# Optimization experiments

Measured on AMD Instinct MI355X. Metric: run time of the kernel, lower is better.

## Reference

```python
import jax, jax.numpy as jnp
import numpy as np

N, E, DIM, H, EDIM = 50000, 800000, 128, 4, 16
C = DIM // H  # per-head channels = 32

def _ln(x, g, b, eps=1e-5):
    mu = jnp.mean(x, -1, keepdims=True)
    var = jnp.mean((x - mu) ** 2, -1, keepdims=True)
    return (x - mu) * jax.lax.rsqrt(var + eps) * g + b

def setup_inputs() -> dict:
    key = jax.random.key(0)
    ks = jax.random.split(key, 16)
    s = lambda d: 1.0 / np.sqrt(d)
    inp = {
        'x': jax.random.normal(ks[0], (N, DIM), jnp.float32),
        'edge_index_s': jax.random.randint(ks[1], (2, E), 0, N, jnp.int64),
        'edge_attr_s': jax.random.normal(ks[2], (E, EDIM), jnp.float32),
        'Wq': jax.random.normal(ks[3], (DIM, DIM), jnp.float32) * s(DIM),
        'bq': jnp.zeros((DIM,), jnp.float32),
        'Wk': jax.random.normal(ks[4], (DIM, DIM), jnp.float32) * s(DIM),
        'bk': jnp.zeros((DIM,), jnp.float32),
        'Wv': jax.random.normal(ks[5], (DIM, DIM), jnp.float32) * s(DIM),
        'bv': jnp.zeros((DIM,), jnp.float32),
        'We': jax.random.normal(ks[6], (EDIM, DIM), jnp.float32) * s(EDIM),
        'be': jnp.zeros((DIM,), jnp.float32),
        'Ws': jax.random.normal(ks[7], (DIM, DIM), jnp.float32) * s(DIM),
        'bs': jnp.zeros((DIM,), jnp.float32),
        'Wbeta': jax.random.normal(ks[8], (3 * DIM, 1), jnp.float32) * s(3 * DIM),
        'g1': jnp.ones((DIM,), jnp.float32),
        'b1': jnp.zeros((DIM,), jnp.float32),
        'Wf1': jax.random.normal(ks[9], (DIM, 4 * DIM), jnp.float32) * s(DIM),
        'bf1': jnp.zeros((4 * DIM,), jnp.float32),
        'Wf2': jax.random.normal(ks[10], (4 * DIM, DIM), jnp.float32) * s(4 * DIM),
        'bf2': jnp.zeros((DIM,), jnp.float32),
        'g2': jnp.ones((DIM,), jnp.float32),
        'b2': jnp.zeros((DIM,), jnp.float32),
    }
    return inp

def reference(x, edge_index_s, edge_attr_s, Wq, bq, Wk, bk, Wv, bv, We, be,
              Ws, bs, Wbeta, g1, b1, Wf1, bf1, Wf2, bf2, g2, b2):
    src, dst = edge_index_s[0], edge_index_s[1]
    # project + reshape to [N, H, C]
    q = (x @ Wq + bq).reshape(N, H, C)
    k = (x @ Wk + bk).reshape(N, H, C)
    v = (x @ Wv + bv).reshape(N, H, C)
    e = (edge_attr_s @ We + be).reshape(E, H, C)
    # gather along edges (irregular access)
    kj = k[src] + e  # [E, H, C]
    vj = v[src] + e
    alpha = jnp.einsum('ehc,ehc->eh', q[dst], kj) / jnp.sqrt(jnp.float32(C))
    # segment softmax over incoming edges of each dst node
    m = jax.ops.segment_max(alpha, dst, num_segments=N)  # [N, H]
    a = jnp.exp(alpha - m[dst])
    denom = jax.ops.segment_sum(a, dst, num_segments=N)
    a = a / (denom[dst] + 1e-16)
    out = jax.ops.segment_sum(a[:, :, None] * vj, dst, num_segments=N)  # [N, H, C]
    out = out.reshape(N, DIM)
    # beta-gated skip (TransformerConv beta=True)
    xr = x @ Ws + bs
    beta = jax.nn.sigmoid(jnp.concatenate([out, xr, out - xr], -1) @ Wbeta)  # [N, 1]
    xs = beta * xr + (1.0 - beta) * out
    # residual + LN + FFN + LN
    h = _ln(x + xs, g1, b1)
    ff = jax.nn.relu(h @ Wf1 + bf1) @ Wf2 + bf2
    return _ln(h + ff, g2, b2)
```

## Files before the change

### kernel.cpp

```cpp
#include <hip/hip_runtime.h>
#include <hip/hip_bf16.h>

#define NN 50000
#define EE 800000
#define DIMM 128

typedef __attribute__((ext_vector_type(8))) short bf16x8;
typedef __attribute__((ext_vector_type(8))) unsigned short us8;
typedef __attribute__((ext_vector_type(4))) float f32x4;

static __device__ __forceinline__ unsigned short f2bf(float f) {
    unsigned int u = __float_as_uint(f);
    unsigned int r = (u + 0x7fffu + ((u >> 16) & 1u)) >> 16;
    return (unsigned short)r;
}
static __device__ __forceinline__ float bf2f(unsigned short s) {
    return __uint_as_float(((unsigned int)s) << 16);
}

__global__ __launch_bounds__(256) void pack_w(
    const float* __restrict__ Wq, const float* __restrict__ Wk,
    const float* __restrict__ Wv, const float* __restrict__ Ws,
    const float* __restrict__ bq, const float* __restrict__ bk,
    const float* __restrict__ bv, const float* __restrict__ bs,
    const float* __restrict__ Wf1, const float* __restrict__ Wf2,
    unsigned short* __restrict__ wqkvsT, unsigned short* __restrict__ wf1T,
    unsigned short* __restrict__ wf2T, float* __restrict__ biasq)
{
    int i = blockIdx.x * 256 + threadIdx.x;
    if (i < 65536) {
        int n = i >> 7, k = i & 127;
        int sel = n >> 7, col = n & 127;
        const float* W = sel == 0 ? Wq : sel == 1 ? Wk : sel == 2 ? Wv : Ws;
        wqkvsT[i] = f2bf(W[k * 128 + col]);
    } else if (i < 131072) {
        int j = i - 65536; int n = j >> 7, k = j & 127;
        wf1T[j] = f2bf(Wf1[k * 512 + n]);
    } else if (i < 196608) {
        int j = i - 131072; int n = j >> 9, k = j & 511;
        wf2T[j] = f2bf(Wf2[k * 128 + n]);
    } else if (i < 196608 + 512) {
        int j = i - 196608; int sel = j >> 7;
        const float* bp = sel == 0 ? bq : sel == 1 ? bk : sel == 2 ? bv : bs;
        biasq[j] = bp[j & 127];
    }
}

template<bool A_BF16, int EPI>
__global__ __launch_bounds__(256) void gemm_k(
    const void* __restrict__ Ap, const unsigned short* __restrict__ Bt,
    const float* __restrict__ bias, void* __restrict__ Cp,
    float* __restrict__ qb, unsigned short* __restrict__ kvb, float* __restrict__ xrb,
    int M, int Nn, int K)
{
    __shared__ unsigned short As[128][72];
    __shared__ unsigned short Bs[64][72];
    int tid = threadIdx.x;
    int nb = Nn >> 6;
    int bm = blockIdx.x / nb, bn = blockIdx.x % nb;
    int w = tid >> 6, lane = tid & 63;
    int wm = w >> 1, wn = w & 1;
    int lr = lane & 15, quad = lane >> 4;

    f32x4 acc[4][2];
    #pragma unroll
    for (int i = 0; i < 4; i++)
        #pragma unroll
        for (int j = 0; j < 2; j++) { f32x4 z = {0.f, 0.f, 0.f, 0.f}; acc[i][j] = z; }

    for (int kc = 0; kc < K; kc += 64) {
        #pragma unroll
        for (int it = 0; it < 4; ++it) {
            int row = it * 32 + (tid >> 3);
            int k8 = (tid & 7) * 8;
            int rg = bm * 128 + row;
            us8 st = {0, 0, 0, 0, 0, 0, 0, 0};
            if (rg < M) {
                if constexpr (A_BF16) {
                    st = *(const us8*)((const unsigned short*)Ap + (size_t)rg * K + kc + k8);
                } else {
                    const float* src = (const float*)Ap + (size_t)rg * K + kc + k8;
                    float4 f0 = *(const float4*)src;
                    float4 f1 = *(const float4*)(src + 4);
                    st[0] = f2bf(f0.x); st[1] = f2bf(f0.y); st[2] = f2bf(f0.z); st[3] = f2bf(f0.w);
                    st[4] = f2bf(f1.x); st[5] = f2bf(f1.y); st[6] = f2bf(f1.z); st[7] = f2bf(f1.w);
                }
            }
            *(us8*)&As[row][k8] = st;
        }
        {
            int nrow = tid >> 2;
            int k16 = (tid & 3) * 16;
            const unsigned short* src = Bt + (size_t)(bn * 64 + nrow) * K + kc + k16;
            *(us8*)&Bs[nrow][k16]     = *(const us8*)src;
            *(us8*)&Bs[nrow][k16 + 8] = *(const us8*)(src + 8);
        }
        __syncthreads();
        #pragma unroll
        for (int kk = 0; kk < 2; ++kk) {
            bf16x8 af[4], bfr[2];
            #pragma unroll
            for (int mi = 0; mi < 4; mi++)
                af[mi] = *(const bf16x8*)&As[wm * 64 + mi * 16 + lr][kk * 32 + quad * 8];
            #pragma unroll
            for (int ni = 0; ni < 2; ni++)
                bfr[ni] = *(const bf16x8*)&Bs[wn * 32 + ni * 16 + lr][kk * 32 + quad * 8];
            #pragma unroll
            for (int mi = 0; mi < 4; mi++)
                #pragma unroll
                for (int ni = 0; ni < 2; ni++)
                    acc[mi][ni] = __builtin_amdgcn_mfma_f32_16x16x32_bf16(af[mi], bfr[ni], acc[mi][ni], 0, 0, 0);
        }
        __syncthreads();
    }
    #pragma unroll
    for (int mi = 0; mi < 4; mi++) {
        #pragma unroll
        for (int ni = 0; ni < 2; ni++) {
            int cg = bn * 64 + wn * 32 + ni * 16 + lr;
            float bv = bias[cg];
            #pragma unroll
            for (int r = 0; r < 4; r++) {
                int rg = bm * 128 + wm * 64 + mi * 16 + quad * 4 + r;
                if (rg < M) {
                    float val = acc[mi][ni][r] + bv;
                    if constexpr (EPI == 0) {
                        ((float*)Cp)[(size_t)rg * Nn + cg] = val;
                    } else if constexpr (EPI == 1) {
                        val = fmaxf(val, 0.f);
                        ((unsigned short*)Cp)[(size_t)rg * Nn + cg] = f2bf(val);
                    } else {
                        int sel = cg >> 7, c = cg & 127;
                        if (sel == 0)      qb[(size_t)rg * 128 + c] = val;
                        else if (sel == 1) kvb[(size_t)rg * 256 + 2 * c] = f2bf(val);
                        else if (sel == 2) kvb[(size_t)rg * 256 + 2 * c + 1] = f2bf(val);
                        else               xrb[(size_t)rg * 128 + c] = val;
                    }
                }
            }
        }
    }
}

__global__ __launch_bounds__(256) void hist_k(const int* __restrict__ dst, int* __restrict__ deg) {
    int e = blockIdx.x * 256 + threadIdx.x;
    if (e < EE) atomicAdd(&deg[dst[e]], 1);
}

__global__ __launch_bounds__(256) void scan_phaseA(const int* __restrict__ deg, int* __restrict__ rs,
                                                   int* __restrict__ bsum) {
    __shared__ int sm[256];
    int tid = threadIdx.x;
    int i = blockIdx.x * 256 + tid;
    int v = (i < NN) ? deg[i] : 0;
    sm[tid] = v;
    __syncthreads();
    #pragma unroll
    for (int off = 1; off < 256; off <<= 1) {
        int t = 0;
        if (tid >= off) t = sm[tid - off];
        __syncthreads();
        if (tid >= off) sm[tid] += t;
        __syncthreads();
    }
    if (i < NN) rs[i] = sm[tid] - v;
    if (tid == 255) bsum[blockIdx.x] = sm[255];
}

__global__ __launch_bounds__(256) void scan_phaseB(int* __restrict__ bsum, int nb) {
    __shared__ int sm[256];
    int tid = threadIdx.x;
    int v = (tid < nb) ? bsum[tid] : 0;
    sm[tid] = v;
    __syncthreads();
    #pragma unroll
    for (int off = 1; off < 256; off <<= 1) {
        int t = 0;
        if (tid >= off) t = sm[tid - off];
        __syncthreads();
        if (tid >= off) sm[tid] += t;
        __syncthreads();
    }
    if (tid < nb) bsum[tid] = sm[tid] - v;
}

__global__ __launch_bounds__(256) void scan_phaseC(int* __restrict__ rs, const int* __restrict__ bsum) {
    int i = blockIdx.x * 256 + threadIdx.x;
    if (i < NN) rs[i] += bsum[blockIdx.x];
    if (i == 0) rs[NN] = EE;
}

__global__ __launch_bounds__(256) void scatter_k(
    const int* __restrict__ src, const int* __restrict__ dst,
    const float* __restrict__ eattr, const int* __restrict__ rs,
    int* __restrict__ cur, int* __restrict__ srcs_sorted,
    unsigned short* __restrict__ eas)
{
    int e = blockIdx.x * 256 + threadIdx.x;
    if (e < EE) {
        int d = dst[e];
        int p = atomicAdd(&cur[d], 1);
        int pos = rs[d] + p;
        srcs_sorted[pos] = src[e];
        const float* ap = eattr + (size_t)e * 16;
        float4 a0 = *(const float4*)ap;
        float4 a1 = *(const float4*)(ap + 4);
        float4 a2 = *(const float4*)(ap + 8);
        float4 a3 = *(const float4*)(ap + 12);
        us8 lo, hi;
        lo[0] = f2bf(a0.x); lo[1] = f2bf(a0.y); lo[2] = f2bf(a0.z); lo[3] = f2bf(a0.w);
        lo[4] = f2bf(a1.x); lo[5] = f2bf(a1.y); lo[6] = f2bf(a1.z); lo[7] = f2bf(a1.w);
        hi[0] = f2bf(a2.x); hi[1] = f2bf(a2.y); hi[2] = f2bf(a2.z); hi[3] = f2bf(a2.w);
        hi[4] = f2bf(a3.x); hi[5] = f2bf(a3.y); hi[6] = f2bf(a3.z); hi[7] = f2bf(a3.w);
        *(us8*)(eas + (size_t)pos * 16)     = lo;
        *(us8*)(eas + (size_t)pos * 16 + 8) = hi;
    }
}

__global__ __launch_bounds__(256, 3) void attn_kernel(
    const float* __restrict__ q, const unsigned int* __restrict__ kvb,
    const float* __restrict__ xr, const float* __restrict__ x,
    const unsigned short* __restrict__ eas, const int* __restrict__ srcs,
    const int* __restrict__ rs,
    const float* __restrict__ We, const float* __restrict__ be,
    const float* __restrict__ Wbeta, const float* __restrict__ gamma1,
    const float* __restrict__ beta1, float* __restrict__ hout)
{
    int wave = threadIdx.x >> 6;
    int lane = threadIdx.x & 63;
    int n = blockIdx.x * 4 + wave;
    if (n >= NN) return;
    int c0 = lane * 2, c1 = c0 + 1;

    float we0[16], we1[16];
    #pragma unroll
    for (int j = 0; j < 16; j++) { we0[j] = We[j * 128 + c0]; we1[j] = We[j * 128 + c1]; }
    float be0 = be[c0], be1 = be[c1];

    float2 q2 = *(const float2*)(q + (size_t)n * 128 + c0);
    q2.x *= 0.17677669529663687f;
    q2.y *= 0.17677669529663687f;

    float l = 0.f, a0 = 0.f, a1 = 0.f;
    int beg = rs[n], end = rs[n + 1];

    const size_t EAS_MAX = (size_t)EE * 16 - 1;
    float ea_c = bf2f(eas[min((size_t)beg * 16 + lane, EAS_MAX)]);
    int sr_c[4];
    #pragma unroll
    for (int j = 0; j < 4; j++) sr_c[j] = srcs[min(beg + j, EE - 1)];

    for (int g = beg; g < end; g += 4) {
        int cnt = end - g;
        uint2 kvp[4];
        #pragma unroll
        for (int j = 0; j < 4; j++)
            kvp[j] = *(const uint2*)(kvb + (size_t)sr_c[j] * 128 + (lane << 1));
        int gn = g + 4;
        float ea_n = bf2f(eas[min((size_t)gn * 16 + lane, EAS_MAX)]);
        int sr_n[4];
        #pragma unroll
        for (int j = 0; j < 4; j++) sr_n[j] = srcs[min(gn + j, EE - 1)];

        #pragma unroll
        for (int j = 0; j < 4; j++) {
            if (j < cnt) {
                float e0 = be0, e1 = be1;
                #pragma unroll
                for (int t = 0; t < 16; t++) {
                    float aa = __shfl(ea_c, j * 16 + t);
                    e0 = fmaf(aa, we0[t], e0);
                    e1 = fmaf(aa, we1[t], e1);
                }
                unsigned int kx = kvp[j].x, ky = kvp[j].y;
                float k0 = __uint_as_float(kx << 16);
                float v0 = __uint_as_float(kx & 0xffff0000u);
                float k1 = __uint_as_float(ky << 16);
                float v1 = __uint_as_float(ky & 0xffff0000u);
                float part = q2.x * (k0 + e0) + q2.y * (k1 + e1);
                part += __shfl_xor(part, 1);
                part += __shfl_xor(part, 2);
                part += __shfl_xor(part, 4);
                part += __shfl_xor(part, 8);
                float wgt = __expf(part);
                l += wgt;
                a0 = fmaf(wgt, v0 + e0, a0);
                a1 = fmaf(wgt, v1 + e1, a1);
            }
        }
        ea_c = ea_n;
        #pragma unroll
        for (int j = 0; j < 4; j++) sr_c[j] = sr_n[j];
    }

    float inv = l > 0.f ? 1.f / l : 0.f;
    float o0 = a0 * inv, o1 = a1 * inv;

    float wbo0 = Wbeta[c0],        wbo1 = Wbeta[c1];
    float wbx0 = Wbeta[128 + c0],  wbx1 = Wbeta[128 + c1];
    float wbd0 = Wbeta[256 + c0],  wbd1 = Wbeta[256 + c1];
    float2 xr2 = *(const float2*)(xr + (size_t)n * 128 + c0);
    float bl = o0 * wbo0 + o1 * wbo1 + xr2.x * wbx0 + xr2.y * wbx1
             + (o0 - xr2.x) * wbd0 + (o1 - xr2.y) * wbd1;
    #pragma unroll
    for (int off = 1; off < 64; off <<= 1) bl += __shfl_xor(bl, off);
    float beta = 1.f / (1.f + __expf(-bl));
    float xs0 = beta * xr2.x + (1.f - beta) * o0;
    float xs1 = beta * xr2.y + (1.f - beta) * o1;

    float2 xv = *(const float2*)(x + (size_t)n * 128 + c0);
    float t0 = xv.x + xs0, t1 = xv.y + xs1;
    float sm = t0 + t1;
    #pragma unroll
    for (int off = 1; off < 64; off <<= 1) sm += __shfl_xor(sm, off);
    float mu = sm * (1.f / 128.f);
    float d0 = t0 - mu, d1 = t1 - mu;
    float vv = d0 * d0 + d1 * d1;
    #pragma unroll
    for (int off = 1; off < 64; off <<= 1) vv += __shfl_xor(vv, off);
    float is = rsqrtf(vv * (1.f / 128.f) + 1e-5f);
    float h0 = d0 * is * gamma1[c0] + beta1[c0];
    float h1 = d1 * is * gamma1[c1] + beta1[c1];
    *(float2*)(hout + (size_t)n * 128 + c0) = make_float2(h0, h1);
}

__global__ __launch_bounds__(256) void ln2_k(
    const float* __restrict__ h, const float* __restrict__ ff2,
    const float* __restrict__ gamma2, const float* __restrict__ beta2,
    float* __restrict__ out)
{
    int wave = threadIdx.x >> 6;
    int lane = threadIdx.x & 63;
    int n = blockIdx.x * 4 + wave;
    if (n >= NN) return;
    int c0 = lane * 2;
    float2 hv = *(const float2*)(h + (size_t)n * 128 + c0);
    float2 fv = *(const float2*)(ff2 + (size_t)n * 128 + c0);
    float t0 = hv.x + fv.x, t1 = hv.y + fv.y;
    float sm = t0 + t1;
    #pragma unroll
    for (int off = 1; off < 64; off <<= 1) sm += __shfl_xor(sm, off);
    float mu = sm * (1.f / 128.f);
    float d0 = t0 - mu, d1 = t1 - mu;
    float vv = d0 * d0 + d1 * d1;
    #pragma unroll
    for (int off = 1; off < 64; off <<= 1) vv += __shfl_xor(vv, off);
    float is = rsqrtf(vv * (1.f / 128.f) + 1e-5f);
    float o0 = d0 * is * gamma2[c0] + beta2[c0];
    float o1 = d1 * is * gamma2[c0 + 1] + beta2[c0 + 1];
    *(float2*)(out + (size_t)n * 128 + c0) = make_float2(o0, o1);
}

extern "C" void kernel_launch(void* const* d_in, const int* in_sizes, int n_in,
                              void* d_out, int out_size, void* d_ws, size_t ws_size,
                              hipStream_t stream) {
    const float* x      = (const float*)d_in[0];
    const int*   eindex = (const int*)d_in[1];
    const float* eattr  = (const float*)d_in[2];
    const float* Wq = (const float*)d_in[3];  const float* bq = (const float*)d_in[4];
    const float* Wk = (const float*)d_in[5];  const float* bk = (const float*)d_in[6];
    const float* Wv = (const float*)d_in[7];  const float* bv = (const float*)d_in[8];
    const float* We = (const float*)d_in[9];  const float* be = (const float*)d_in[10];
    const float* Ws = (const float*)d_in[11]; const float* bs = (const float*)d_in[12];
    const float* Wbeta = (const float*)d_in[13];
    const float* g1 = (const float*)d_in[14]; const float* b1 = (const float*)d_in[15];
    const float* Wf1 = (const float*)d_in[16]; const float* bf1 = (const float*)d_in[17];
    const float* Wf2 = (const float*)d_in[18]; const float* bf2 = (const float*)d_in[19];
    const float* g2 = (const float*)d_in[20]; const float* b2 = (const float*)d_in[21];

    char* ws = (char*)d_ws;
    size_t off = 0;
    unsigned short* wqkvsT = (unsigned short*)(ws + off); off += 512 * 128 * 2;
    unsigned short* wf1T   = (unsigned short*)(ws + off); off += 512 * 128 * 2;
    unsigned short* wf2T   = (unsigned short*)(ws + off); off += 128 * 512 * 2;
    float* biasq           = (float*)(ws + off);          off += 512 * 4;
    float* qb              = (float*)(ws + off);          off += (size_t)NN * 128 * 4;
    unsigned short* kvb    = (unsigned short*)(ws + off); off += (size_t)NN * 256 * 2;
    float* xrb             = (float*)(ws + off);          off += (size_t)NN * 128 * 4;
    float* h               = (float*)(ws + off);          off += (size_t)NN * 128 * 4;
    unsigned short* ff1    = (unsigned short*)(ws + off); off += (size_t)NN * 512 * 2;
    float* ff2             = (float*)(ws + off);          off += (size_t)NN * 128 * 4;
    int* deg               = (int*)(ws + off);            off += NN * 4;
    int* cursor            = (int*)(ws + off);            off += NN * 4;
    int* row_start         = (int*)(ws + off);            off += (NN + 1) * 4;
    int* bsum              = (int*)(ws + off);            off += 256 * 4;
    int* srcs_sorted       = (int*)(ws + off);            off += (size_t)EE * 4;
    unsigned short* eas    = (unsigned short*)(ws + off); off += (size_t)EE * 16 * 2;

    hipMemsetAsync(deg, 0, 2 * NN * 4, stream);

    pack_w<<<770, 256, 0, stream>>>(Wq, Wk, Wv, Ws, bq, bk, bv, bs, Wf1, Wf2,
                                    wqkvsT, wf1T, wf2T, biasq);

    gemm_k<false, 2><<<391 * 8, 256, 0, stream>>>(x, wqkvsT, biasq, nullptr,
                                                  qb, kvb, xrb, NN, 512, 128);

    hist_k<<<3125, 256, 0, stream>>>(eindex + EE, deg);
    scan_phaseA<<<196, 256, 0, stream>>>(deg, row_start, bsum);
    scan_phaseB<<<1, 256, 0, stream>>>(bsum, 196);
    scan_phaseC<<<196, 256, 0, stream>>>(row_start, bsum);
    scatter_k<<<3125, 256, 0, stream>>>(eindex, eindex + EE, eattr, row_start,
                                        cursor, srcs_sorted, eas);

    attn_kernel<<<12500, 256, 0, stream>>>(qb, (const unsigned int*)kvb, xrb, x,
                                           eas, srcs_sorted, row_start,
                                           We, be, Wbeta, g1, b1, h);

    gemm_k<false, 1><<<391 * 8, 256, 0, stream>>>(h, wf1T, bf1, ff1,
                                                  nullptr, nullptr, nullptr, NN, 512, 128);
    gemm_k<true, 0><<<391 * 2, 256, 0, stream>>>(ff1, wf2T, bf2, ff2,
                                                 nullptr, nullptr, nullptr, NN, 128, 512);

    ln2_k<<<12500, 256, 0, stream>>>(h, ff2, g2, b2, (float*)d_out);
}
```

Before: 581.3 us.

## Factor edge projection out of attention loop and feed FFN1 bf16 activations

The attention kernel stops rebuilding the 128-wide edge embedding per edge. Scores now use precomputed q·We and q·be terms. The weighted sum of raw 16-dim edge attributes is accumulated and projected through We once per node, and the edge batch grows from 4 to 8 per iteration. The kernel also writes a bf16 copy of h so the first FFN GEMM reads bf16 directly instead of converting fp32, and workspace buffers are aliased and 256-byte aligned. This removes most per-edge shuffles and FMAs, at the cost of more registers for the deeper prefetch and a changed rounding order in the softmax accumulation.

```diff
diff --git a/kernel.cpp b/kernel.cpp
--- a/kernel.cpp
+++ b/kernel.cpp
@@ -39,7 +39,7 @@
     } else if (i < 196608) {
         int j = i - 131072; int n = j >> 9, k = j & 511;
         wf2T[j] = f2bf(Wf2[k * 128 + n]);
-    } else if (i < 196608 + 512) {
+    } else if (i < 197120) {
         int j = i - 196608; int sel = j >> 7;
         const float* bp = sel == 0 ? bq : sel == 1 ? bk : sel == 2 ? bv : bs;
         biasq[j] = bp[j & 127];
@@ -223,14 +223,17 @@
     const unsigned short* __restrict__ eas, const int* __restrict__ srcs,
     const int* __restrict__ rs,
     const float* __restrict__ We, const float* __restrict__ be,
-    const float* __restrict__ Wbeta, const float* __restrict__ gamma1,
-    const float* __restrict__ beta1, float* __restrict__ hout)
+    const float* __restrict__ Wbeta,
+    const float* __restrict__ gamma1, const float* __restrict__ beta1,
+    float* __restrict__ hout, unsigned int* __restrict__ hbf)
 {
     int wave = threadIdx.x >> 6;
     int lane = threadIdx.x & 63;
     int n = blockIdx.x * 4 + wave;
     if (n >= NN) return;
     int c0 = lane * 2, c1 = c0 + 1;
+    int jlane = lane & 15;
+    int hbase = lane & 48;
 
     float we0[16], we1[16];
     #pragma unroll
@@ -241,57 +244,75 @@
     q2.x *= 0.17677669529663687f;
     q2.y *= 0.17677669529663687f;
 
-    float l = 0.f, a0 = 0.f, a1 = 0.f;
+    float qbe = q2.x * be0 + q2.y * be1;
+    qbe += __shfl_xor(qbe, 1); qbe += __shfl_xor(qbe, 2);
+    qbe += __shfl_xor(qbe, 4); qbe += __shfl_xor(qbe, 8);
+    float qwe = 0.f;
+    #pragma unroll
+    for (int j = 0; j < 16; j++) {
+        float u = q2.x * we0[j] + q2.y * we1[j];
+        u += __shfl_xor(u, 1); u += __shfl_xor(u, 2);
+        u += __shfl_xor(u, 4); u += __shfl_xor(u, 8);
+        if (jlane == j) qwe = u;
+    }
+
+    float l = 0.f, a0 = 0.f, a1 = 0.f, s = 0.f;
     int beg = rs[n], end = rs[n + 1];
 
-    const size_t EAS_MAX = (size_t)EE * 16 - 1;
-    float ea_c = bf2f(eas[min((size_t)beg * 16 + lane, EAS_MAX)]);
-    int sr_c[4];
-    #pragma unroll
-    for (int j = 0; j < 4; j++) sr_c[j] = srcs[min(beg + j, EE - 1)];
-
-    for (int g = beg; g < end; g += 4) {
+    int sr_c[8]; unsigned short e_c[8];
+    #pragma unroll
+    for (int j = 0; j < 8; j++) {
+        int idx = min(beg + j, EE - 1);
+        sr_c[j] = srcs[idx];
+        e_c[j] = eas[(size_t)idx * 16 + jlane];
+    }
+    for (int g = beg; g < end; g += 8) {
+        uint2 kvp[8];
+        #pragma unroll
+        for (int j = 0; j < 8; j++)
+            kvp[j] = *(const uint2*)(kvb + (size_t)sr_c[j] * 128 + (lane << 1));
+        int gn = g + 8;
+        int sr_n[8]; unsigned short e_n[8];
+        #pragma unroll
+        for (int j = 0; j < 8; j++) {
+            int idx = min(gn + j, EE - 1);
+            sr_n[j] = srcs[idx];
+            e_n[j] = eas[(size_t)idx * 16 + jlane];
+        }
         int cnt = end - g;
-        uint2 kvp[4];
-        #pragma unroll
-        for (int j = 0; j < 4; j++)
-            kvp[j] = *(const uint2*)(kvb + (size_t)sr_c[j] * 128 + (lane << 1));
-        int gn = g + 4;
-        float ea_n = bf2f(eas[min((size_t)gn * 16 + lane, EAS_MAX)]);
-        int sr_n[4];
-        #pragma unroll
-        for (int j = 0; j < 4; j++) sr_n[j] = srcs[min(gn + j, EE - 1)];
-
-        #pragma unroll
-        for (int j = 0; j < 4; j++) {
+        #pragma unroll
+        for (int j = 0; j < 8; j++) {
             if (j < cnt) {
-                float e0 = be0, e1 = be1;
-                #pragma unroll
-                for (int t = 0; t < 16; t++) {
-                    float aa = __shfl(ea_c, j * 16 + t);
-                    e0 = fmaf(aa, we0[t], e0);
-                    e1 = fmaf(aa, we1[t], e1);
-                }
+                float ea = bf2f(e_c[j]);
                 unsigned int kx = kvp[j].x, ky = kvp[j].y;
                 float k0 = __uint_as_float(kx << 16);
                 float v0 = __uint_as_float(kx & 0xffff0000u);
                 float k1 = __uint_as_float(ky << 16);
                 float v1 = __uint_as_float(ky & 0xffff0000u);
-                float part = q2.x * (k0 + e0) + q2.y * (k1 + e1);
+                float part = fmaf(q2.x, k0, fmaf(q2.y, k1, qwe * ea));
                 part += __shfl_xor(part, 1);
                 part += __shfl_xor(part, 2);
                 part += __shfl_xor(part, 4);
                 part += __shfl_xor(part, 8);
-                float wgt = __expf(part);
+                float wgt = __expf(part + qbe);
                 l += wgt;
-                a0 = fmaf(wgt, v0 + e0, a0);
-                a1 = fmaf(wgt, v1 + e1, a1);
+                a0 = fmaf(wgt, v0, a0);
+                a1 = fmaf(wgt, v1, a1);
+                s = fmaf(wgt, ea, s);
             }
         }
-        ea_c = ea_n;
-        #pragma unroll
-        for (int j = 0; j < 4; j++) sr_c[j] = sr_n[j];
-    }
+        #pragma unroll
+        for (int j = 0; j < 8; j++) { sr_c[j] = sr_n[j]; e_c[j] = e_n[j]; }
+    }
+
+    float eo0 = l * be0, eo1 = l * be1;
+    #pragma unroll
+    for (int j = 0; j < 16; j++) {
+        float sj = __shfl(s, hbase + j);
+        eo0 = fmaf(sj, we0[j], eo0);
+        eo1 = fmaf(sj, we1[j], eo1);
+    }
+    a0 += eo0; a1 += eo1;
 
     float inv = l > 0.f ? 1.f / l : 0.f;
     float o0 = a0 * inv, o1 = a1 * inv;
@@ -322,6 +343,7 @@
     float h0 = d0 * is * gamma1[c0] + beta1[c0];
     float h1 = d1 * is * gamma1[c1] + beta1[c1];
     *(float2*)(hout + (size_t)n * 128 + c0) = make_float2(h0, h1);
+    hbf[(size_t)n * 64 + lane] = (unsigned int)f2bf(h0) | ((unsigned int)f2bf(h1) << 16);
 }
 
 __global__ __launch_bounds__(256) void ln2_k(
@@ -370,24 +392,27 @@
 
     char* ws = (char*)d_ws;
     size_t off = 0;
-    unsigned short* wqkvsT = (unsigned short*)(ws + off); off += 512 * 128 * 2;
-    unsigned short* wf1T   = (unsigned short*)(ws + off); off += 512 * 128 * 2;
-    unsigned short* wf2T   = (unsigned short*)(ws + off); off += 128 * 512 * 2;
-    float* biasq           = (float*)(ws + off);          off += 512 * 4;
-    float* qb              = (float*)(ws + off);          off += (size_t)NN * 128 * 4;
-    unsigned short* kvb    = (unsigned short*)(ws + off); off += (size_t)NN * 256 * 2;
-    float* xrb             = (float*)(ws + off);          off += (size_t)NN * 128 * 4;
-    float* h               = (float*)(ws + off);          off += (size_t)NN * 128 * 4;
-    unsigned short* ff1    = (unsigned short*)(ws + off); off += (size_t)NN * 512 * 2;
-    float* ff2             = (float*)(ws + off);          off += (size_t)NN * 128 * 4;
-    int* deg               = (int*)(ws + off);            off += NN * 4;
-    int* cursor            = (int*)(ws + off);            off += NN * 4;
-    int* row_start         = (int*)(ws + off);            off += (NN + 1) * 4;
-    int* bsum              = (int*)(ws + off);            off += 256 * 4;
-    int* srcs_sorted       = (int*)(ws + off);            off += (size_t)EE * 4;
-    unsigned short* eas    = (unsigned short*)(ws + off); off += (size_t)EE * 16 * 2;
-
-    hipMemsetAsync(deg, 0, 2 * NN * 4, stream);
+    #define ALLOC(ptr, type, bytes) type* ptr = (type*)(ws + off); off = (off + (size_t)(bytes) + 255) & ~(size_t)255;
+    ALLOC(wqkvsT, unsigned short, 512 * 128 * 2)
+    ALLOC(wf1T,   unsigned short, 512 * 128 * 2)
+    ALLOC(wf2T,   unsigned short, 128 * 512 * 2)
+    ALLOC(biasq,  float,          512 * 4)
+    ALLOC(qb,     float,          (size_t)NN * 128 * 4)
+    ALLOC(kvb,    unsigned short, (size_t)NN * 256 * 2)
+    ALLOC(xrb,    float,          (size_t)NN * 128 * 4)
+    ALLOC(h,      float,          (size_t)NN * 128 * 4)
+    ALLOC(hbf,    unsigned int,   (size_t)NN * 128 * 2)
+    ALLOC(deg,    int,            2 * NN * 4)
+    ALLOC(row_start, int,         (NN + 1) * 4)
+    ALLOC(bsum,   int,            1024)
+    ALLOC(srcs_sorted, int,       (size_t)EE * 4)
+    ALLOC(eas,    unsigned short, (size_t)EE * 16 * 2)
+    #undef ALLOC
+    int* cursor = deg + NN;
+    unsigned short* ff1 = (unsigned short*)qb;
+    float* ff2 = xrb;
+
+    hipMemsetAsync(deg, 0, (size_t)2 * NN * 4, stream);
 
     pack_w<<<770, 256, 0, stream>>>(Wq, Wk, Wv, Ws, bq, bk, bv, bs, Wf1, Wf2,
                                     wqkvsT, wf1T, wf2T, biasq);
@@ -404,10 +429,10 @@
 
     attn_kernel<<<12500, 256, 0, stream>>>(qb, (const unsigned int*)kvb, xrb, x,
                                            eas, srcs_sorted, row_start,
-                                           We, be, Wbeta, g1, b1, h);
-
-    gemm_k<false, 1><<<391 * 8, 256, 0, stream>>>(h, wf1T, bf1, ff1,
-                                                  nullptr, nullptr, nullptr, NN, 512, 128);
+                                           We, be, Wbeta, g1, b1, h, hbf);
+
+    gemm_k<true, 1><<<391 * 8, 256, 0, stream>>>(hbf, wf1T, bf1, ff1,
+                                                 nullptr, nullptr, nullptr, NN, 512, 128);
     gemm_k<true, 0><<<391 * 2, 256, 0, stream>>>(ff1, wf2T, bf2, ff2,
                                                  nullptr, nullptr, nullptr, NN, 128, 512);
 
```

Result: faster. 527.0 us (-9.3%).
